# Kernel tuning notes

Hardware: AMD Instinct MI355X
Metric: run time of the kernel (lower is better)

The kernel has to match this reference:

```python
import jax, jax.numpy as jnp
import numpy as np


def _conv1x1(x, w, b):
    # x: [B, Cin, H, W], w: [Cout, Cin], b: [Cout]
    return jnp.einsum('bchw,oc->bohw', x, w) + b[None, :, None, None]


def setup_inputs() -> dict:
    key = jax.random.key(0)
    ks = jax.random.split(key, 9)
    B, C, H, W = 32, 512, 32, 32
    Cout, dn = 512, 512
    s_in = 1.0 / np.sqrt(C)
    s_out = 1.0 / np.sqrt(Cout)
    return {
        'x': jax.random.normal(ks[0], (B, C, H, W), jnp.float32),
        'wA': jax.random.uniform(ks[1], (Cout, C), jnp.float32, -s_in, s_in),
        'bA': jax.random.uniform(ks[2], (Cout,), jnp.float32, -s_in, s_in),
        'wB': jax.random.uniform(ks[3], (dn, C), jnp.float32, -s_in, s_in),
        'bB': jax.random.uniform(ks[4], (dn,), jnp.float32, -s_in, s_in),
        'wV': jax.random.uniform(ks[5], (dn, C), jnp.float32, -s_in, s_in),
        'bV': jax.random.uniform(ks[6], (dn,), jnp.float32, -s_in, s_in),
        'wR': jax.random.uniform(ks[7], (Cout, Cout), jnp.float32, -s_out, s_out),
        'bR': jax.random.uniform(ks[8], (Cout,), jnp.float32, -s_out, s_out),
    }


def reference(x, wA, bA, wB, bB, wV, bV, wR, bR):
    Bsz, C, H, W = x.shape
    Cout = wA.shape[0]
    A = _conv1x1(x, wA, bA).reshape(Bsz, Cout, H * W)          # [B, Cout, N]
    Bm = _conv1x1(x, wB, bB).reshape(Bsz, wB.shape[0], H * W)  # [B, dn, N]
    Vm = _conv1x1(x, wV, bV).reshape(Bsz, wV.shape[0], H * W)  # [B, dn, N]
    attn_maps = jax.nn.softmax(Bm, axis=-1)                    # softmax over spatial
    attn_vectors = jax.nn.softmax(Vm, axis=-1)                 # softmax over spatial
    glob_desc = jnp.einsum('bcn,bdn->bcd', A, attn_maps)       # [B, Cout, dn]
    Z = jnp.einsum('bcd,bdn->bcn', glob_desc, attn_vectors)    # [B, Cout, N]
    Z = Z.reshape(Bsz, Cout, H, W)
    Z = _conv1x1(Z, wR, bR)
    return Z
```

## Files before the change

### kernel.cpp

```cpp
#include <hip/hip_runtime.h>
#include <stdint.h>

typedef unsigned short u16;
typedef __bf16  bf16x8 __attribute__((ext_vector_type(8)));
typedef float   f32x4  __attribute__((ext_vector_type(4)));

__device__ __forceinline__ u16 f2bf(float f) {
    union { float f; unsigned u; } c; c.f = f;
    unsigned r = c.u + 0x7fffu + ((c.u >> 16) & 1u);
    return (u16)(r >> 16);
}
__device__ __forceinline__ float bf2f(u16 b) {
    union { unsigned u; float f; } c; c.u = ((unsigned)b) << 16; return c.f;
}

__device__ __forceinline__ void g2l16(const u16* g, u16* l) {
    __builtin_amdgcn_global_load_lds(
        (__attribute__((address_space(1))) void*)(uintptr_t)g,
        (__attribute__((address_space(3))) void*)(uint32_t)(uintptr_t)l,
        16, 0, 0);
}

template <int TM, bool HAS_BIAS, bool OUT_F32, bool EPI, bool CSCALE>
__device__ __forceinline__ void gemm_core(
    const u16* __restrict__ Ab, const u16* __restrict__ Bb, void* __restrict__ C,
    const float* __restrict__ bias, int N, int K, long cbase, int m0, int n0,
    const float* __restrict__ svec, const float* __restrict__ wRbA,
    const float* __restrict__ rs)
{
    constexpr int MI = TM / 32;
    constexpr int NA = TM / 32;
    __shared__ __align__(16) u16 As[TM * 64];
    __shared__ __align__(16) u16 Bs[128 * 64];

    const int t = threadIdx.x;
    const int w = t >> 6, lane = t & 63;
    const int wr = w >> 1, wc = w & 1;

    f32x4 acc[MI][4];
    const f32x4 zero = {0.f, 0.f, 0.f, 0.f};
#pragma unroll
    for (int i = 0; i < MI; ++i)
#pragma unroll
        for (int j = 0; j < 4; ++j) acc[i][j] = zero;

    int  aslot[NA]; long aoff[NA];
#pragma unroll
    for (int i = 0; i < NA; ++i) {
        const int s   = i * 256 + t;
        const int row = s >> 3;
        const int col = ((s & 7) ^ (row & 7)) * 8;
        aslot[i] = s * 8;
        aoff[i]  = (long)(m0 + row) * K + col;
    }
    int  bslot[4]; long boff[4];
#pragma unroll
    for (int i = 0; i < 4; ++i) {
        const int s   = i * 256 + t;
        const int row = s >> 3;
        const int col = ((s & 7) ^ (row & 7)) * 8;
        bslot[i] = s * 8;
        boff[i]  = (long)(n0 + row) * K + col;
    }

    const int fr = lane & 15;
    const int q  = lane >> 4;
    const int o0 = ((q ^ (fr & 7)) * 8);
    const u16* fa = &As[(wr * (TM / 2) + fr) * 64];
    const u16* fb = &Bs[(wc * 64 + fr) * 64];

    for (int k0 = 0; k0 < K; k0 += 64) {
#pragma unroll
        for (int i = 0; i < NA; ++i) g2l16(Ab + aoff[i] + k0, &As[aslot[i]]);
#pragma unroll
        for (int i = 0; i < 4; ++i)  g2l16(Bb + boff[i] + k0, &Bs[bslot[i]]);
        __syncthreads();

#pragma unroll
        for (int kh = 0; kh < 2; ++kh) {
            const int o = o0 ^ (kh * 32);
            bf16x8 af[MI], bv[4];
#pragma unroll
            for (int mi = 0; mi < MI; ++mi) af[mi] = *(const bf16x8*)(fa + mi * 1024 + o);
#pragma unroll
            for (int ni = 0; ni < 4; ++ni)  bv[ni] = *(const bf16x8*)(fb + ni * 1024 + o);
#pragma unroll
            for (int mi = 0; mi < MI; ++mi)
#pragma unroll
                for (int ni = 0; ni < 4; ++ni)
                    acc[mi][ni] = __builtin_amdgcn_mfma_f32_16x16x32_bf16(
                        af[mi], bv[ni], acc[mi][ni], 0, 0, 0);
        }
        __syncthreads();
    }

    const int ccol  = n0 + wc * 64 + fr;
    const int crow0 = m0 + wr * (TM / 2) + (lane >> 4) * 4;
    float se[4], sc[4];
    if (EPI) {
#pragma unroll
        for (int ni = 0; ni < 4; ++ni) se[ni] = svec[ccol + ni * 16];
    }
    if (CSCALE) {
#pragma unroll
        for (int ni = 0; ni < 4; ++ni) {
            const int c = ccol + ni * 16;
            const float sb = rs[c]       + rs[1024 + c] + rs[2048 + c] + rs[3072 + c];
            const float sv = rs[512 + c] + rs[1536 + c] + rs[2560 + c] + rs[3584 + c];
            sc[ni] = 1.0f / (sb * sv);
        }
    }
#pragma unroll
    for (int mi = 0; mi < MI; ++mi) {
#pragma unroll
        for (int r = 0; r < 4; ++r) {
            const int row = crow0 + mi * 16 + r;
            float add = HAS_BIAS ? bias[row] : 0.f;
            float rk  = EPI ? wRbA[row] : 0.f;
#pragma unroll
            for (int ni = 0; ni < 4; ++ni) {
                float v = acc[mi][ni][r] + add;
                if (CSCALE) v *= sc[ni];
                if (EPI)    v += rk * se[ni];
                const long idx = cbase + (long)row * N + ccol + ni * 16;
                if (OUT_F32) ((float*)C)[idx] = v;
                else         ((u16*)C)[idx]   = f2bf(v);
            }
        }
    }
}

template <int TM, bool HAS_BIAS, bool OUT_F32>
__global__ __launch_bounds__(256) void gemm_nt(
    const u16* __restrict__ A, const u16* __restrict__ B, void* __restrict__ C,
    const float* __restrict__ bias, int N, int K, long sA, long sB, long sC)
{
    const int bz = blockIdx.z;
    gemm_core<TM, HAS_BIAS, OUT_F32, false, false>(
        A + (long)bz * sA, B + (long)bz * sB, C, bias, N, K,
        (long)bz * sC, blockIdx.y * TM, blockIdx.x * 128, nullptr, nullptr, nullptr);
}

template <int TM, bool HAS_BIAS, bool OUT_F32, bool EPI, bool CSCALE>
__global__ __launch_bounds__(256) void gemm_nt_swz(
    const u16* __restrict__ A, const u16* __restrict__ B, void* __restrict__ C,
    const float* __restrict__ bias, int N, int K, long sA, long sB, long sC,
    int bxn, int bpb, const float* __restrict__ s_all,
    const float* __restrict__ wRbA, const float* __restrict__ rs_all)
{
    const int blk  = blockIdx.x;
    const int xcd  = blk & 7;
    const int slot = blk >> 3;
    const int b    = xcd + 8 * (slot / bpb);
    const int wi   = slot % bpb;
    const int bx   = wi % bxn;
    const int by   = wi / bxn;
    gemm_core<TM, HAS_BIAS, OUT_F32, EPI, CSCALE>(
        A + (long)b * sA, B + (long)b * sB, C, bias, N, K,
        (long)b * sC, by * TM, bx * 128,
        EPI ? s_all + (long)b * 1024 : nullptr, wRbA,
        CSCALE ? rs_all + (long)b * 4096 : nullptr);
}

__global__ __launch_bounds__(512) void gemm2_y(
    const u16* __restrict__ A,
    const u16* __restrict__ B,
    u16* __restrict__ C,
    const float* __restrict__ bias,
    float* __restrict__ rspart)
{
    constexpr int K    = 512;
    constexpr int NT   = K / 32;
    constexpr int AREG = 256 * 32;
    constexpr int BUFQ = 2 * AREG;
    __shared__ __align__(16) u16 lds[4 * BUFQ];

    const int blk  = blockIdx.x;
    const int xcd  = blk & 7;
    const int slot = blk >> 3;
    const int bz   = xcd + 8 * (slot / 24);
    const int wi   = slot % 24;
    const int m0   = (wi >> 2) * 256;
    const int n0   = (wi & 3) * 256;

    const u16* Ab = A;
    const u16* Bb = B + (long)bz * (1024 * 512);
    u16*       Cb = C + (long)bz * ((long)1536 * 1024);

    const int t    = threadIdx.x;
    const int w    = t >> 6, lane = t & 63;
    const int wr   = w >> 2, wc = w & 3;
    const int fr   = lane & 15, q = lane >> 4;

    int  aslot[2]; long agoff[2], bgoff[2];
#pragma unroll
    for (int i = 0; i < 2; ++i) {
        const int ci  = i * 512 + t;
        const int row = ci >> 2;
        const int gc  = (ci & 3) ^ ((row >> 1) & 3);
        aslot[i] = ci * 8;
        agoff[i] = (long)(m0 + row) * K + gc * 8;
        bgoff[i] = (long)(n0 + row) * K + gc * 8;
    }

    const int rchunk = (q ^ ((fr >> 1) & 3)) * 8;
    const int abase  = (wr * 128 + fr) * 32 + rchunk;
    const int bbase  = (wc * 64  + fr) * 32 + rchunk;

    f32x4 acc[8][4];
    const f32x4 zero = {0.f, 0.f, 0.f, 0.f};
#pragma unroll
    for (int i = 0; i < 8; ++i)
#pragma unroll
        for (int j = 0; j < 4; ++j) acc[i][j] = zero;

#pragma unroll
    for (int i = 0; i < 2; ++i) g2l16(Ab + agoff[i],        &lds[aslot[i]]);
#pragma unroll
    for (int i = 0; i < 2; ++i) g2l16(Bb + bgoff[i],        &lds[AREG + aslot[i]]);
#pragma unroll
    for (int i = 0; i < 2; ++i) g2l16(Ab + agoff[i] + 32,   &lds[BUFQ + aslot[i]]);
#pragma unroll
    for (int i = 0; i < 2; ++i) g2l16(Bb + bgoff[i] + 32,   &lds[BUFQ + AREG + aslot[i]]);
    asm volatile("s_waitcnt vmcnt(4)" ::: "memory");
    __builtin_amdgcn_s_barrier();
    asm volatile("" ::: "memory");

#pragma unroll
    for (int kt = 0; kt < NT; ++kt) {
        const u16* Abuf = &lds[(kt & 3) * BUFQ];
        const u16* Bbuf = Abuf + AREG;
        u16* dst = &lds[((kt + 2) & 3) * BUFQ];
        const long kg = (long)(kt + 2) * 32;

        bf16x8 av[8], bv[4];
#pragma unroll
        for (int mi = 0; mi < 8; ++mi) av[mi] = *(const bf16x8*)(Abuf + abase + mi * 512);
#pragma unroll
        for (int ni = 0; ni < 4; ++ni) bv[ni] = *(const bf16x8*)(Bbuf + bbase + ni * 512);
        if (kt + 2 < NT) {
#pragma unroll
            for (int i = 0; i < 2; ++i) g2l16(Ab + agoff[i] + kg, dst + aslot[i]);
#pragma unroll
            for (int i = 0; i < 2; ++i) g2l16(Bb + bgoff[i] + kg, dst + AREG + aslot[i]);
        }
#pragma unroll
        for (int mi = 0; mi < 8; ++mi)
#pragma unroll
            for (int ni = 0; ni < 4; ++ni)
                acc[mi][ni] = __builtin_amdgcn_mfma_f32_16x16x32_bf16(
                    av[mi], bv[ni], acc[mi][ni], 0, 0, 0);

        if (kt + 1 < NT) {
            if (kt + 2 < NT) asm volatile("s_waitcnt vmcnt(4)" ::: "memory");
            else             asm volatile("s_waitcnt vmcnt(0)" ::: "memory");
            __builtin_amdgcn_s_barrier();
            asm volatile("" ::: "memory");
        }
    }

    const int ccol  = n0 + wc * 64 + fr;
    const int crow0 = m0 + wr * 128 + q * 4;
    const bool sm = (m0 >= 512);
    float rsums[8][4];
#pragma unroll
    for (int mi = 0; mi < 8; ++mi) {
#pragma unroll
        for (int r = 0; r < 4; ++r) {
            const int row = crow0 + mi * 16 + r;
            const float add = bias[row];
            float rsum = 0.f;
#pragma unroll
            for (int ni = 0; ni < 4; ++ni) {
                float v = acc[mi][ni][r] + add;
                if (sm) { v = __expf(v); rsum += v; }
                Cb[(long)row * 1024 + ccol + ni * 16] = f2bf(v);
            }
            rsums[mi][r] = rsum;
        }
    }
    if (sm) {
#pragma unroll
        for (int mi = 0; mi < 8; ++mi)
#pragma unroll
            for (int r = 0; r < 4; ++r) {
                float v = rsums[mi][r];
                v += __shfl_xor(v, 1);
                v += __shfl_xor(v, 2);
                v += __shfl_xor(v, 4);
                v += __shfl_xor(v, 8);
                rsums[mi][r] = v;
            }
        __syncthreads();
        float* lsc = (float*)lds;
        if (fr == 0) {
#pragma unroll
            for (int mi = 0; mi < 8; ++mi)
#pragma unroll
                for (int r = 0; r < 4; ++r) {
                    const int lrow = mi * 16 + q * 4 + r;
                    lsc[(wr * 128 + lrow) * 4 + wc] = rsums[mi][r];
                }
        }
        __syncthreads();
        if (t < 256) {
            const f32x4 pv = *(const f32x4*)&lsc[t * 4];
            const int grow = (m0 - 512) + t;
            rspart[((long)bz * 4 + (n0 >> 8)) * 1024 + grow] =
                pv[0] + pv[1] + pv[2] + pv[3];
        }
    }
}

__global__ __launch_bounds__(256) void cast_transpose_x(
    const float* __restrict__ in, u16* __restrict__ out)
{
    __shared__ u16 tile[64][68];
    const int bz = blockIdx.z;
    const float* ip = in  + (long)bz * (512 * 1024);
    u16*         op = out + (long)bz * (1024 * 512);
    const int c0 = blockIdx.x * 64;
    const int r0 = blockIdx.y * 64;
    const int tx = threadIdx.x & 15;
    const int ty = threadIdx.x >> 4;
#pragma unroll
    for (int p = 0; p < 4; ++p) {
        const int row = ty + 16 * p;
        float4 v = *(const float4*)(ip + (long)(r0 + row) * 1024 + c0 + 4 * tx);
        ushort4 o;
        o.x = f2bf(v.x); o.y = f2bf(v.y); o.z = f2bf(v.z); o.w = f2bf(v.w);
        *(ushort4*)&tile[row][4 * tx] = o;
    }
    __syncthreads();
#pragma unroll
    for (int p = 0; p < 4; ++p) {
        const int orow = ty + 16 * p;
        ushort4 o;
        o.x = tile[4 * tx + 0][orow];
        o.y = tile[4 * tx + 1][orow];
        o.z = tile[4 * tx + 2][orow];
        o.w = tile[4 * tx + 3][orow];
        *(ushort4*)&op[(long)(c0 + orow) * 512 + r0 + 4 * tx] = o;
    }
}

__global__ __launch_bounds__(256) void transpose_colsum(
    const u16* __restrict__ in, u16* __restrict__ out, float* __restrict__ s,
    long sIn, long sOut, const float* __restrict__ rspart)
{
    __shared__ u16 tile[64][68];
    __shared__ float sinv[64];
    const int bz = blockIdx.z;
    const u16* ip = in  + (long)bz * sIn;
    u16*       op = out + (long)bz * sOut;
    const int c0 = blockIdx.x * 64;
    const int r0 = blockIdx.y * 64;
    const int t  = threadIdx.x;
    const int tx = t & 15;
    const int ty = t >> 4;
    if (t < 64) {
        const float* rs = rspart + (long)bz * 4096 + 512 + r0 + t;
        sinv[t] = 1.0f / (rs[0] + rs[1024] + rs[2048] + rs[3072]);
    }
#pragma unroll
    for (int p = 0; p < 4; ++p) {
        const int row = ty + 16 * p;
        ushort4 v = *(const ushort4*)(ip + (long)(r0 + row) * 1024 + c0 + 4 * tx);
        *(ushort4*)&tile[row][4 * tx] = v;
    }
    __syncthreads();
#pragma unroll
    for (int p = 0; p < 4; ++p) {
        const int orow = ty + 16 * p;
        ushort4 o;
        o.x = tile[4 * tx + 0][orow];
        o.y = tile[4 * tx + 1][orow];
        o.z = tile[4 * tx + 2][orow];
        o.w = tile[4 * tx + 3][orow];
        *(ushort4*)&op[(long)(c0 + orow) * 512 + r0 + 4 * tx] = o;
    }
    if (t < 64) {
        float a = 0.f;
#pragma unroll 8
        for (int d = 0; d < 64; ++d) a += bf2f(tile[d][t]) * sinv[d];
        atomicAdd(&s[(long)bz * 1024 + c0 + t], a);
    }
}

__global__ __launch_bounds__(256) void prep_weights(
    const float* __restrict__ wA, const float* __restrict__ wB,
    const float* __restrict__ wV, const float* __restrict__ wR,
    const float* __restrict__ bA, const float* __restrict__ bB,
    const float* __restrict__ bV,
    u16* __restrict__ Wcat, u16* __restrict__ wRb, u16* __restrict__ wAtb,
    float* __restrict__ bcat, float* __restrict__ wRbA,
    float* __restrict__ svec)
{
    const int blk = blockIdx.x;
    if (blk < 4103) {
        const int tid = blk * 256 + threadIdx.x;
        if (tid < 262144) {
            Wcat[262144 + tid] = f2bf(wB[tid]);
        } else if (tid < 524288) {
            Wcat[262144 + tid] = f2bf(wV[tid - 262144]);
        } else if (tid < 786432) {
            wRb[tid - 524288] = f2bf(wR[tid - 524288]);
        } else if (tid < 1048576) {
            const int i = tid - 786432;
            wAtb[(i & 511) * 512 + (i >> 9)] = f2bf(wA[i]);
        } else if (tid < 1048576 + 1536) {
            const int j = tid - 1048576;
            bcat[j] = (j < 512) ? 0.f : (j < 1024) ? bB[j - 512] : bV[j - 1024];
        }
    } else if (blk < 4231) {
        const int o    = (blk - 4103) * 4 + (threadIdx.x >> 6);
        const int lane = threadIdx.x & 63;
        float a = 0.f;
#pragma unroll
        for (int c = lane; c < 512; c += 64) a += wR[o * 512 + c] * bA[c];
#pragma unroll
        for (int off = 32; off > 0; off >>= 1) a += __shfl_down(a, off);
        if (lane == 0) wRbA[o] = a;
    } else {
        svec[(blk - 4231) * 256 + threadIdx.x] = 0.f;
    }
}

extern "C" void kernel_launch(void* const* d_in, const int* in_sizes, int n_in,
                              void* d_out, int out_size, void* d_ws, size_t ws_size,
                              hipStream_t stream)
{
    (void)in_sizes; (void)n_in; (void)out_size; (void)ws_size;
    const float* x  = (const float*)d_in[0];
    const float* wA = (const float*)d_in[1];
    const float* bA = (const float*)d_in[2];
    const float* wB = (const float*)d_in[3];
    const float* bB = (const float*)d_in[4];
    const float* wV = (const float*)d_in[5];
    const float* bV = (const float*)d_in[6];
    const float* wR = (const float*)d_in[7];
    const float* bR = (const float*)d_in[8];
    float* out = (float*)d_out;

    const int B = 32;
    const long sY = (long)1536 * 1024;

    char* p = (char*)d_ws;
    u16*   Y    = (u16*)p;   p += (long)B * sY * 2;
    u16*   H    = (u16*)p;   p += (long)B * 512 * 512 * 2;
    u16*   Wcat = (u16*)p;   p += (long)1536 * 512 * 2;
    u16*   wRb  = (u16*)p;   p += (long)512 * 512 * 2;
    u16*   wAtb = (u16*)p;   p += (long)512 * 512 * 2;
    float* bcat = (float*)p; p += 1536 * 4;
    float* svec = (float*)p; p += (long)B * 1024 * 4;
    float* wRbA = (float*)p; p += 512 * 4;
    float* rspart = (float*)p; p += (long)B * 4096 * 4;

    u16* Xt = (u16*)d_out;
    u16* Vt = Y;

    cast_transpose_x<<<dim3(16, 8, B), 256, 0, stream>>>(x, Xt);
    prep_weights<<<dim3(4359), 256, 0, stream>>>(wA, wB, wV, wR, bA, bB, bV,
                                                 Wcat, wRb, wAtb, bcat, wRbA,
                                                 svec);

    gemm_nt<128, false, false><<<dim3(4, 4, 1), 256, 0, stream>>>(
        wRb, wAtb, Wcat, nullptr, 512, 512, 0, 0, 0);

    gemm2_y<<<dim3(768), 512, 0, stream>>>(Wcat, Xt, Y, bcat, rspart);

    gemm_nt_swz<128, false, false, false, true><<<dim3(512), 256, 0, stream>>>(
        Y, Y + (long)512 * 1024, H, nullptr, 512, 1024,
        sY, sY, (long)512 * 512, 4, 16, nullptr, nullptr, rspart);

    transpose_colsum<<<dim3(16, 8, B), 256, 0, stream>>>(
        Y + (long)1024 * 1024, Vt, svec, sY, sY, rspart);

    gemm_nt_swz<128, true, true, true, false><<<dim3(1024), 256, 0, stream>>>(
        H, Vt, out, bR, 1024, 512, (long)512 * 512, sY, (long)512 * 1024,
        8, 32, svec, wRbA, nullptr);
}
```

Before: 280.8 us.

## Fuse V transpose into GEMM epilogue and fold bias term into H scaling

The V-branch GEMM epilogue now writes exp values directly in transposed layout, which removes the separate transpose_colsum kernel. The rank-1 bias correction (wR·bA times the column sums of normalized V) is moved into the H GEMM epilogue as an extra wRbA/sv term, so the final GEMM epilogue only adds the bias. The x cast-transpose and weight prep are merged into one launch. This cuts two kernel launches, one full read and write of V, and the atomics, at the cost of strided 8-byte stores of transposed V in gemm2_y.

```diff
diff --git a/kernel.cpp b/kernel.cpp
--- a/kernel.cpp
+++ b/kernel.cpp
@@ -21,11 +21,11 @@
         16, 0, 0);
 }
 
-template <int TM, bool HAS_BIAS, bool OUT_F32, bool EPI, bool CSCALE>
+template <int TM, bool HAS_BIAS, bool OUT_F32, bool CSCALE>
 __device__ __forceinline__ void gemm_core(
     const u16* __restrict__ Ab, const u16* __restrict__ Bb, void* __restrict__ C,
     const float* __restrict__ bias, int N, int K, long cbase, int m0, int n0,
-    const float* __restrict__ svec, const float* __restrict__ wRbA,
+    const float* __restrict__ wRbA,
     const float* __restrict__ rs)
 {
     constexpr int MI = TM / 32;
@@ -96,18 +96,15 @@
 
     const int ccol  = n0 + wc * 64 + fr;
     const int crow0 = m0 + wr * (TM / 2) + (lane >> 4) * 4;
-    float se[4], sc[4];
-    if (EPI) {
-#pragma unroll
-        for (int ni = 0; ni < 4; ++ni) se[ni] = svec[ccol + ni * 16];
-    }
+    float sc[4], svn[4];
     if (CSCALE) {
 #pragma unroll
         for (int ni = 0; ni < 4; ++ni) {
             const int c = ccol + ni * 16;
             const float sb = rs[c]       + rs[1024 + c] + rs[2048 + c] + rs[3072 + c];
             const float sv = rs[512 + c] + rs[1536 + c] + rs[2560 + c] + rs[3584 + c];
-            sc[ni] = 1.0f / (sb * sv);
+            sc[ni]  = 1.0f / (sb * sv);
+            svn[ni] = 1.0f / sv;
         }
     }
 #pragma unroll
@@ -116,12 +113,11 @@
         for (int r = 0; r < 4; ++r) {
             const int row = crow0 + mi * 16 + r;
             float add = HAS_BIAS ? bias[row] : 0.f;
-            float rk  = EPI ? wRbA[row] : 0.f;
+            float rk  = CSCALE ? wRbA[row] : 0.f;
 #pragma unroll
             for (int ni = 0; ni < 4; ++ni) {
                 float v = acc[mi][ni][r] + add;
-                if (CSCALE) v *= sc[ni];
-                if (EPI)    v += rk * se[ni];
+                if (CSCALE) v = v * sc[ni] + rk * svn[ni];
                 const long idx = cbase + (long)row * N + ccol + ni * 16;
                 if (OUT_F32) ((float*)C)[idx] = v;
                 else         ((u16*)C)[idx]   = f2bf(v);
@@ -136,17 +132,17 @@
     const float* __restrict__ bias, int N, int K, long sA, long sB, long sC)
 {
     const int bz = blockIdx.z;
-    gemm_core<TM, HAS_BIAS, OUT_F32, false, false>(
+    gemm_core<TM, HAS_BIAS, OUT_F32, false>(
         A + (long)bz * sA, B + (long)bz * sB, C, bias, N, K,
-        (long)bz * sC, blockIdx.y * TM, blockIdx.x * 128, nullptr, nullptr, nullptr);
-}
-
-template <int TM, bool HAS_BIAS, bool OUT_F32, bool EPI, bool CSCALE>
+        (long)bz * sC, blockIdx.y * TM, blockIdx.x * 128, nullptr, nullptr);
+}
+
+template <int TM, bool HAS_BIAS, bool OUT_F32, bool CSCALE>
 __global__ __launch_bounds__(256) void gemm_nt_swz(
     const u16* __restrict__ A, const u16* __restrict__ B, void* __restrict__ C,
     const float* __restrict__ bias, int N, int K, long sA, long sB, long sC,
-    int bxn, int bpb, const float* __restrict__ s_all,
-    const float* __restrict__ wRbA, const float* __restrict__ rs_all)
+    int bxn, int bpb, const float* __restrict__ wRbA,
+    const float* __restrict__ rs_all)
 {
     const int blk  = blockIdx.x;
     const int xcd  = blk & 7;
@@ -155,10 +151,9 @@
     const int wi   = slot % bpb;
     const int bx   = wi % bxn;
     const int by   = wi / bxn;
-    gemm_core<TM, HAS_BIAS, OUT_F32, EPI, CSCALE>(
+    gemm_core<TM, HAS_BIAS, OUT_F32, CSCALE>(
         A + (long)b * sA, B + (long)b * sB, C, bias, N, K,
-        (long)b * sC, by * TM, bx * 128,
-        EPI ? s_all + (long)b * 1024 : nullptr, wRbA,
+        (long)b * sC, by * TM, bx * 128, wRbA,
         CSCALE ? rs_all + (long)b * 4096 : nullptr);
 }
 
@@ -262,21 +257,44 @@
     const int ccol  = n0 + wc * 64 + fr;
     const int crow0 = m0 + wr * 128 + q * 4;
     const bool sm = (m0 >= 512);
+    const bool tr = (m0 >= 1024);
     float rsums[8][4];
-#pragma unroll
-    for (int mi = 0; mi < 8; ++mi) {
-#pragma unroll
-        for (int r = 0; r < 4; ++r) {
-            const int row = crow0 + mi * 16 + r;
-            const float add = bias[row];
-            float rsum = 0.f;
+    if (!tr) {
+#pragma unroll
+        for (int mi = 0; mi < 8; ++mi) {
+#pragma unroll
+            for (int r = 0; r < 4; ++r) {
+                const int row = crow0 + mi * 16 + r;
+                const float add = bias[row];
+                float rsum = 0.f;
+#pragma unroll
+                for (int ni = 0; ni < 4; ++ni) {
+                    float v = acc[mi][ni][r] + add;
+                    if (sm) { v = __expf(v); rsum += v; }
+                    Cb[(long)row * 1024 + ccol + ni * 16] = f2bf(v);
+                }
+                rsums[mi][r] = rsum;
+            }
+        }
+    } else {
+        u16* Vtb = Cb + (long)1024 * 1024;
+#pragma unroll
+        for (int mi = 0; mi < 8; ++mi) {
+            const int growr = crow0 + mi * 16;
+            const int d0    = growr - 1024;
+#pragma unroll
+            for (int r = 0; r < 4; ++r) rsums[mi][r] = 0.f;
 #pragma unroll
             for (int ni = 0; ni < 4; ++ni) {
-                float v = acc[mi][ni][r] + add;
-                if (sm) { v = __expf(v); rsum += v; }
-                Cb[(long)row * 1024 + ccol + ni * 16] = f2bf(v);
+                const int n = ccol + ni * 16;
+                ushort4 o4;
+                float e;
+                e = __expf(acc[mi][ni][0] + bias[growr + 0]); rsums[mi][0] += e; o4.x = f2bf(e);
+                e = __expf(acc[mi][ni][1] + bias[growr + 1]); rsums[mi][1] += e; o4.y = f2bf(e);
+                e = __expf(acc[mi][ni][2] + bias[growr + 2]); rsums[mi][2] += e; o4.z = f2bf(e);
+                e = __expf(acc[mi][ni][3] + bias[growr + 3]); rsums[mi][3] += e; o4.w = f2bf(e);
+                *(ushort4*)&Vtb[(long)n * 512 + d0] = o4;
             }
-            rsums[mi][r] = rsum;
         }
     }
     if (sm) {
@@ -312,93 +330,47 @@
     }
 }
 
-__global__ __launch_bounds__(256) void cast_transpose_x(
-    const float* __restrict__ in, u16* __restrict__ out)
-{
-    __shared__ u16 tile[64][68];
-    const int bz = blockIdx.z;
-    const float* ip = in  + (long)bz * (512 * 1024);
-    u16*         op = out + (long)bz * (1024 * 512);
-    const int c0 = blockIdx.x * 64;
-    const int r0 = blockIdx.y * 64;
-    const int tx = threadIdx.x & 15;
-    const int ty = threadIdx.x >> 4;
-#pragma unroll
-    for (int p = 0; p < 4; ++p) {
-        const int row = ty + 16 * p;
-        float4 v = *(const float4*)(ip + (long)(r0 + row) * 1024 + c0 + 4 * tx);
-        ushort4 o;
-        o.x = f2bf(v.x); o.y = f2bf(v.y); o.z = f2bf(v.z); o.w = f2bf(v.w);
-        *(ushort4*)&tile[row][4 * tx] = o;
-    }
-    __syncthreads();
-#pragma unroll
-    for (int p = 0; p < 4; ++p) {
-        const int orow = ty + 16 * p;
-        ushort4 o;
-        o.x = tile[4 * tx + 0][orow];
-        o.y = tile[4 * tx + 1][orow];
-        o.z = tile[4 * tx + 2][orow];
-        o.w = tile[4 * tx + 3][orow];
-        *(ushort4*)&op[(long)(c0 + orow) * 512 + r0 + 4 * tx] = o;
-    }
-}
-
-__global__ __launch_bounds__(256) void transpose_colsum(
-    const u16* __restrict__ in, u16* __restrict__ out, float* __restrict__ s,
-    long sIn, long sOut, const float* __restrict__ rspart)
-{
-    __shared__ u16 tile[64][68];
-    __shared__ float sinv[64];
-    const int bz = blockIdx.z;
-    const u16* ip = in  + (long)bz * sIn;
-    u16*       op = out + (long)bz * sOut;
-    const int c0 = blockIdx.x * 64;
-    const int r0 = blockIdx.y * 64;
-    const int t  = threadIdx.x;
-    const int tx = t & 15;
-    const int ty = t >> 4;
-    if (t < 64) {
-        const float* rs = rspart + (long)bz * 4096 + 512 + r0 + t;
-        sinv[t] = 1.0f / (rs[0] + rs[1024] + rs[2048] + rs[3072]);
-    }
-#pragma unroll
-    for (int p = 0; p < 4; ++p) {
-        const int row = ty + 16 * p;
-        ushort4 v = *(const ushort4*)(ip + (long)(r0 + row) * 1024 + c0 + 4 * tx);
-        *(ushort4*)&tile[row][4 * tx] = v;
-    }
-    __syncthreads();
-#pragma unroll
-    for (int p = 0; p < 4; ++p) {
-        const int orow = ty + 16 * p;
-        ushort4 o;
-        o.x = tile[4 * tx + 0][orow];
-        o.y = tile[4 * tx + 1][orow];
-        o.z = tile[4 * tx + 2][orow];
-        o.w = tile[4 * tx + 3][orow];
-        *(ushort4*)&op[(long)(c0 + orow) * 512 + r0 + 4 * tx] = o;
-    }
-    if (t < 64) {
-        float a = 0.f;
-#pragma unroll 8
-        for (int d = 0; d < 64; ++d) a += bf2f(tile[d][t]) * sinv[d];
-        atomicAdd(&s[(long)bz * 1024 + c0 + t], a);
-    }
-}
-
-__global__ __launch_bounds__(256) void prep_weights(
+__global__ __launch_bounds__(256) void fused_pre(
+    const float* __restrict__ in, u16* __restrict__ out,
     const float* __restrict__ wA, const float* __restrict__ wB,
     const float* __restrict__ wV, const float* __restrict__ wR,
     const float* __restrict__ bA, const float* __restrict__ bB,
     const float* __restrict__ bV,
     u16* __restrict__ Wcat, u16* __restrict__ wRb, u16* __restrict__ wAtb,
-    float* __restrict__ bcat, float* __restrict__ wRbA,
-    float* __restrict__ svec)
-{
+    float* __restrict__ bcat, float* __restrict__ wRbA)
+{
+    __shared__ u16 tile[64][68];
     const int blk = blockIdx.x;
-    if (blk < 4103) {
-        const int tid = blk * 256 + threadIdx.x;
+    if (blk < 4096) {
+        const int bz  = blk >> 7;
+        const int rem = blk & 127;
+        const int c0  = (rem & 15) * 64;
+        const int r0  = (rem >> 4) * 64;
+        const float* ip = in  + (long)bz * (512 * 1024);
+        u16*         op = out + (long)bz * (1024 * 512);
+        const int tx = threadIdx.x & 15;
+        const int ty = threadIdx.x >> 4;
+#pragma unroll
+        for (int p = 0; p < 4; ++p) {
+            const int row = ty + 16 * p;
+            float4 v = *(const float4*)(ip + (long)(r0 + row) * 1024 + c0 + 4 * tx);
+            ushort4 o;
+            o.x = f2bf(v.x); o.y = f2bf(v.y); o.z = f2bf(v.z); o.w = f2bf(v.w);
+            *(ushort4*)&tile[row][4 * tx] = o;
+        }
+        __syncthreads();
+#pragma unroll
+        for (int p = 0; p < 4; ++p) {
+            const int orow = ty + 16 * p;
+            ushort4 o;
+            o.x = tile[4 * tx + 0][orow];
+            o.y = tile[4 * tx + 1][orow];
+            o.z = tile[4 * tx + 2][orow];
+            o.w = tile[4 * tx + 3][orow];
+            *(ushort4*)&op[(long)(c0 + orow) * 512 + r0 + 4 * tx] = o;
+        }
+    } else if (blk < 4096 + 4103) {
+        const int tid = (blk - 4096) * 256 + threadIdx.x;
         if (tid < 262144) {
             Wcat[262144 + tid] = f2bf(wB[tid]);
         } else if (tid < 524288) {
@@ -412,8 +384,8 @@
             const int j = tid - 1048576;
             bcat[j] = (j < 512) ? 0.f : (j < 1024) ? bB[j - 512] : bV[j - 1024];
         }
-    } else if (blk < 4231) {
-        const int o    = (blk - 4103) * 4 + (threadIdx.x >> 6);
+    } else {
+        const int o    = (blk - (4096 + 4103)) * 4 + (threadIdx.x >> 6);
         const int lane = threadIdx.x & 63;
         float a = 0.f;
 #pragma unroll
@@ -421,8 +393,6 @@
 #pragma unroll
         for (int off = 32; off > 0; off >>= 1) a += __shfl_down(a, off);
         if (lane == 0) wRbA[o] = a;
-    } else {
-        svec[(blk - 4231) * 256 + threadIdx.x] = 0.f;
     }
 }
 
@@ -452,31 +422,24 @@
     u16*   wRb  = (u16*)p;   p += (long)512 * 512 * 2;
     u16*   wAtb = (u16*)p;   p += (long)512 * 512 * 2;
     float* bcat = (float*)p; p += 1536 * 4;
-    float* svec = (float*)p; p += (long)B * 1024 * 4;
     float* wRbA = (float*)p; p += 512 * 4;
     float* rspart = (float*)p; p += (long)B * 4096 * 4;
 
     u16* Xt = (u16*)d_out;
-    u16* Vt = Y;
-
-    cast_transpose_x<<<dim3(16, 8, B), 256, 0, stream>>>(x, Xt);
-    prep_weights<<<dim3(4359), 256, 0, stream>>>(wA, wB, wV, wR, bA, bB, bV,
-                                                 Wcat, wRb, wAtb, bcat, wRbA,
-                                                 svec);
+
+    fused_pre<<<dim3(8327), 256, 0, stream>>>(x, Xt, wA, wB, wV, wR, bA, bB, bV,
+                                              Wcat, wRb, wAtb, bcat, wRbA);
 
     gemm_nt<128, false, false><<<dim3(4, 4, 1), 256, 0, stream>>>(
         wRb, wAtb, Wcat, nullptr, 512, 512, 0, 0, 0);
 
     gemm2_y<<<dim3(768), 512, 0, stream>>>(Wcat, Xt, Y, bcat, rspart);
 
-    gemm_nt_swz<128, false, false, false, true><<<dim3(512), 256, 0, stream>>>(
+    gemm_nt_swz<128, false, false, true><<<dim3(512), 256, 0, stream>>>(
         Y, Y + (long)512 * 1024, H, nullptr, 512, 1024,
-        sY, sY, (long)512 * 512, 4, 16, nullptr, nullptr, rspart);
-
-    transpose_colsum<<<dim3(16, 8, B), 256, 0, stream>>>(
-        Y + (long)1024 * 1024, Vt, svec, sY, sY, rspart);
-
-    gemm_nt_swz<128, true, true, true, false><<<dim3(1024), 256, 0, stream>>>(
-        H, Vt, out, bR, 1024, 512, (long)512 * 512, sY, (long)512 * 1024,
-        8, 32, svec, wRbA, nullptr);
-}
+        sY, sY, (long)512 * 512, 4, 16, wRbA, rspart);
+
+    gemm_nt_swz<128, true, true, false><<<dim3(1024), 256, 0, stream>>>(
+        H, Y + (long)1024 * 1024, out, bR, 1024, 512,
+        (long)512 * 512, sY, (long)512 * 1024, 8, 32, nullptr, nullptr);
+}
```

Result: faster. 267.7 us (-4.7%).
